# Kernel tuning notes

Hardware: AMD Instinct MI355X
Metric: run time of the kernel (lower is better)

Reference implementation:

```python
import jax, jax.numpy as jnp
import numpy as np

D_MODEL = 1024
KEY_MODEL = 1024
D_K = 64
D_V = 64
N_HEAD = 8
PROJ = N_HEAD * D_V  # 512


def setup_inputs() -> dict:
    key = jax.random.key(0)
    ks = jax.random.split(key, 9)
    N, M = 8192, 8192
    s = 0.02
    return {
        "q": jax.random.normal(ks[0], (N, D_MODEL), jnp.float32),
        "k": jax.random.normal(ks[1], (M, KEY_MODEL), jnp.float32),
        "v": jax.random.normal(ks[2], (M, D_MODEL), jnp.float32),
        "Wq": jax.random.normal(ks[3], (D_MODEL, PROJ), jnp.float32) * s,
        "bq": jnp.zeros((PROJ,), jnp.float32),
        "Wk": jax.random.normal(ks[4], (KEY_MODEL, PROJ), jnp.float32) * s,
        "bk": jnp.zeros((PROJ,), jnp.float32),
        "Wv": jax.random.normal(ks[5], (D_MODEL, PROJ), jnp.float32) * s,
        "bv": jnp.zeros((PROJ,), jnp.float32),
    }


def reference(q, k, v, Wq, bq, Wk, bk, Wv, bv):
    # Linear projections (torch nn.Linear: x @ W^T + b; here W stored as [in,out])
    qp = q @ Wq + bq                      # [N, PROJ]
    kp = k @ Wk + bk                      # [M, PROJ]
    vp = v @ Wv + bv                      # [M, PROJ]
    # Note: original scales by d_k (NOT sqrt(d_k)); dropout is identity at eval.
    scores = (qp @ kp.T) / D_K            # [N, M]
    attn = jax.nn.softmax(scores, axis=-1)
    return attn @ vp                      # [N, PROJ]
```

## Files before the change

kernel.cpp:

```cpp
#include <hip/hip_runtime.h>
#include <hip/hip_bf16.h>
#include <stdint.h>
#include <stddef.h>

typedef unsigned short u16;
typedef short bf16x8 __attribute__((ext_vector_type(8)));
typedef short bf16x4 __attribute__((ext_vector_type(4)));
typedef float floatx4 __attribute__((ext_vector_type(4)));

#define N_ROWS 8192
#define D_MODEL 1024
#define PROJ 512
#define MHALF 4096
#define SCALE_LOG2E_DK 0.022542110013890054f

__device__ __forceinline__ float bf2f(u16 u) {
    union { unsigned int i; float f; } x; x.i = ((unsigned int)u) << 16; return x.f;
}
__device__ __forceinline__ u16 f2bf(float f) {
    __hip_bfloat16 h = __float2bfloat16(f);
    return *reinterpret_cast<u16*>(&h);
}

__global__ void transpose_w_kernel(const float* __restrict__ in, u16* __restrict__ out,
                                   int R, int C) {
    __shared__ u16 tile[32][33];
    int r = blockIdx.y * 32 + threadIdx.y;
    int c = blockIdx.x * 32 + threadIdx.x;
    tile[threadIdx.y][threadIdx.x] = f2bf(in[(size_t)r * C + c]);
    __syncthreads();
    int ro = blockIdx.x * 32 + threadIdx.y;
    int co = blockIdx.y * 32 + threadIdx.x;
    out[(size_t)ro * R + co] = tile[threadIdx.x][threadIdx.y];
}

__global__ void transpose_kernel(const u16* __restrict__ in, u16* __restrict__ out,
                                 int R, int C) {
    __shared__ u16 tile[32][33];
    int r = blockIdx.y * 32 + threadIdx.y;
    int c = blockIdx.x * 32 + threadIdx.x;
    tile[threadIdx.y][threadIdx.x] = in[(size_t)r * C + c];
    __syncthreads();
    int ro = blockIdx.x * 32 + threadIdx.y;
    int co = blockIdx.y * 32 + threadIdx.x;
    out[(size_t)ro * R + co] = tile[threadIdx.x][threadIdx.y];
}

__global__ __launch_bounds__(256) void proj_kernel(
    const float* __restrict__ qin, const float* __restrict__ kin, const float* __restrict__ vin,
    const u16* __restrict__ WqT, const u16* __restrict__ WkT, const u16* __restrict__ WvT,
    const float* __restrict__ bq, const float* __restrict__ bk, const float* __restrict__ bv,
    u16* __restrict__ qp, u16* __restrict__ kp, u16* __restrict__ vp)
{
    const int z = blockIdx.z;
    const float* A    = (z == 0) ? qin : (z == 1) ? kin : vin;
    const u16* WT     = (z == 0) ? WqT : (z == 1) ? WkT : WvT;
    const float* bias = (z == 0) ? bq  : (z == 1) ? bk  : bv;
    u16* C            = (z == 0) ? qp  : (z == 1) ? kp  : vp;

    const int m0 = blockIdx.x * 128;
    const int n0 = blockIdx.y * 128;
    __shared__ __align__(16) u16 smem[2 * 128 * 40];
    u16* As = smem;
    u16* Bs = smem + 128 * 40;

    const int t = threadIdx.x;
    const int w = t >> 6, l = t & 63;
    const int q16 = l >> 4, l16 = l & 15;
    const int wm = (w & 1) * 64, wn = (w >> 1) * 64;

    floatx4 acc[4][4] = {};

    for (int k0 = 0; k0 < D_MODEL; k0 += 32) {
        __syncthreads();
#pragma unroll
        for (int i = 0; i < 4; ++i) {
            int id = i * 256 + t;
            int r = id >> 3, c = id & 7;
            float4 f = *(const float4*)(A + (size_t)(m0 + r) * D_MODEL + k0 + c * 4);
            bf16x4 hv;
            hv[0] = (short)f2bf(f.x); hv[1] = (short)f2bf(f.y);
            hv[2] = (short)f2bf(f.z); hv[3] = (short)f2bf(f.w);
            *(bf16x4*)(As + r * 40 + c * 4) = hv;
        }
#pragma unroll
        for (int i = 0; i < 2; ++i) {
            int id = i * 256 + t;
            int r = id >> 2, c = id & 3;
            *(bf16x8*)(Bs + r * 40 + c * 8) =
                *(const bf16x8*)(WT + (size_t)(n0 + r) * D_MODEL + k0 + c * 8);
        }
        __syncthreads();

        bf16x8 af[4], bfr[4];
#pragma unroll
        for (int mi = 0; mi < 4; ++mi)
            af[mi] = *(const bf16x8*)(As + (wm + mi * 16 + l16) * 40 + q16 * 8);
#pragma unroll
        for (int ni = 0; ni < 4; ++ni)
            bfr[ni] = *(const bf16x8*)(Bs + (wn + ni * 16 + l16) * 40 + q16 * 8);
#pragma unroll
        for (int mi = 0; mi < 4; ++mi)
#pragma unroll
            for (int ni = 0; ni < 4; ++ni)
                acc[mi][ni] = __builtin_amdgcn_mfma_f32_16x16x32_bf16(
                    af[mi], bfr[ni], acc[mi][ni], 0, 0, 0);
    }

#pragma unroll
    for (int ni = 0; ni < 4; ++ni) {
        int col = n0 + wn + ni * 16 + l16;
        float bv_ = bias[col];
#pragma unroll
        for (int mi = 0; mi < 4; ++mi)
#pragma unroll
            for (int rr = 0; rr < 4; ++rr) {
                int row = m0 + wm + mi * 16 + q16 * 4 + rr;
                C[(size_t)row * PROJ + col] = f2bf(acc[mi][ni][rr] + bv_);
            }
    }
}

__global__ void zero_l_kernel(float* __restrict__ l) {
    l[blockIdx.x * 256 + threadIdx.x] = 0.f;
}

__global__ __launch_bounds__(256) void score_kernel(
    const u16* __restrict__ qp, const u16* __restrict__ kph,
    u16* __restrict__ P, float* __restrict__ l)
{
    const int m0 = blockIdx.x * 128;
    const int n0 = blockIdx.y * 128;
    __shared__ __align__(16) u16 smem[2 * 128 * 40];
    u16* As = smem;
    u16* Bs = smem + 128 * 40;

    const int t = threadIdx.x;
    const int w = t >> 6, lane = t & 63;
    const int q16 = lane >> 4, l16 = lane & 15;
    const int wm = (w & 1) * 64, wn = (w >> 1) * 64;

    floatx4 acc[4][4] = {};

    for (int k0 = 0; k0 < PROJ; k0 += 32) {
        __syncthreads();
#pragma unroll
        for (int i = 0; i < 2; ++i) {
            int id = i * 256 + t;
            int r = id >> 2, c = id & 3;
            *(bf16x8*)(As + r * 40 + c * 8) =
                *(const bf16x8*)(qp + (size_t)(m0 + r) * PROJ + k0 + c * 8);
            *(bf16x8*)(Bs + r * 40 + c * 8) =
                *(const bf16x8*)(kph + (size_t)(n0 + r) * PROJ + k0 + c * 8);
        }
        __syncthreads();

        bf16x8 af[4], bfr[4];
#pragma unroll
        for (int mi = 0; mi < 4; ++mi)
            af[mi] = *(const bf16x8*)(As + (wm + mi * 16 + l16) * 40 + q16 * 8);
#pragma unroll
        for (int ni = 0; ni < 4; ++ni)
            bfr[ni] = *(const bf16x8*)(Bs + (wn + ni * 16 + l16) * 40 + q16 * 8);
#pragma unroll
        for (int mi = 0; mi < 4; ++mi)
#pragma unroll
            for (int ni = 0; ni < 4; ++ni)
                acc[mi][ni] = __builtin_amdgcn_mfma_f32_16x16x32_bf16(
                    af[mi], bfr[ni], acc[mi][ni], 0, 0, 0);
    }

#pragma unroll
    for (int mi = 0; mi < 4; ++mi)
#pragma unroll
        for (int rr = 0; rr < 4; ++rr) {
            int row = m0 + wm + mi * 16 + q16 * 4 + rr;
            u16* Prow = P + (size_t)row * MHALF + n0 + wn;
            float tot = 0.f;
#pragma unroll
            for (int ni = 0; ni < 4; ++ni) {
                float x = acc[mi][ni][rr] * SCALE_LOG2E_DK;
                x = fminf(fmaxf(x, -30.f), 30.f);
                float p = exp2f(x);
                tot += p;
                Prow[ni * 16 + l16] = f2bf(p);
            }
#pragma unroll
            for (int m = 1; m < 16; m <<= 1)
                tot += __shfl_xor(tot, m, 64);
            if (l16 == 0)
                atomicAdd(&l[row], tot);
        }
}

__global__ __launch_bounds__(256) void pv_kernel(
    const u16* __restrict__ P, const u16* __restrict__ vpTh,
    float* __restrict__ Ofull, u16* __restrict__ Opart, int accum)
{
    const int m0 = blockIdx.x * 128;
    const int n0 = blockIdx.y * 128;
    const int kg = blockIdx.z;
    const int kbase = kg * 2048;
    __shared__ __align__(16) u16 smem[2 * 128 * 40];
    u16* As = smem;
    u16* Bs = smem + 128 * 40;

    const int t = threadIdx.x;
    const int w = t >> 6, lane = t & 63;
    const int q16 = lane >> 4, l16 = lane & 15;
    const int wm = (w & 1) * 64, wn = (w >> 1) * 64;

    floatx4 acc[4][4] = {};

    for (int kk = 0; kk < 2048; kk += 32) {
        const int k0 = kbase + kk;
        __syncthreads();
#pragma unroll
        for (int i = 0; i < 2; ++i) {
            int id = i * 256 + t;
            int r = id >> 2, c = id & 3;
            *(bf16x8*)(As + r * 40 + c * 8) =
                *(const bf16x8*)(P + (size_t)(m0 + r) * MHALF + k0 + c * 8);
            *(bf16x8*)(Bs + r * 40 + c * 8) =
                *(const bf16x8*)(vpTh + (size_t)(n0 + r) * N_ROWS + k0 + c * 8);
        }
        __syncthreads();

        bf16x8 af[4], bfr[4];
#pragma unroll
        for (int mi = 0; mi < 4; ++mi)
            af[mi] = *(const bf16x8*)(As + (wm + mi * 16 + l16) * 40 + q16 * 8);
#pragma unroll
        for (int ni = 0; ni < 4; ++ni)
            bfr[ni] = *(const bf16x8*)(Bs + (wn + ni * 16 + l16) * 40 + q16 * 8);
#pragma unroll
        for (int mi = 0; mi < 4; ++mi)
#pragma unroll
            for (int ni = 0; ni < 4; ++ni)
                acc[mi][ni] = __builtin_amdgcn_mfma_f32_16x16x32_bf16(
                    af[mi], bfr[ni], acc[mi][ni], 0, 0, 0);
    }

#pragma unroll
    for (int ni = 0; ni < 4; ++ni) {
        int col = n0 + wn + ni * 16 + l16;
#pragma unroll
        for (int mi = 0; mi < 4; ++mi)
#pragma unroll
            for (int rr = 0; rr < 4; ++rr) {
                int row = m0 + wm + mi * 16 + q16 * 4 + rr;
                size_t o = (size_t)row * PROJ + col;
                float v = acc[mi][ni][rr];
                if (kg == 0) {
                    if (accum) v += Ofull[o];
                    Ofull[o] = v;
                } else {
                    if (accum) v += bf2f(Opart[o]);
                    Opart[o] = f2bf(v);
                }
            }
    }
}

__global__ void scale_kernel(float* __restrict__ out, const u16* __restrict__ Opart,
                             const float* __restrict__ l)
{
    int idx = blockIdx.x * 256 + threadIdx.x;
    int row = idx >> 9;
    out[idx] = (out[idx] + bf2f(Opart[idx])) / l[row];
}

extern "C" void kernel_launch(void* const* d_in, const int* in_sizes, int n_in,
                              void* d_out, int out_size, void* d_ws, size_t ws_size,
                              hipStream_t stream)
{
    (void)in_sizes; (void)n_in; (void)out_size;
    if (ws_size < ((size_t)101 << 20)) return;

    const float* q  = (const float*)d_in[0];
    const float* k  = (const float*)d_in[1];
    const float* v  = (const float*)d_in[2];
    const float* Wq = (const float*)d_in[3];
    const float* bq = (const float*)d_in[4];
    const float* Wk = (const float*)d_in[5];
    const float* bk = (const float*)d_in[6];
    const float* Wv = (const float*)d_in[7];
    const float* bv = (const float*)d_in[8];

    char* ws = (char*)d_ws;
    u16* qp    = (u16*)(ws);
    u16* kp    = (u16*)(ws + ((size_t)8  << 20));
    u16* vp    = (u16*)(ws + ((size_t)16 << 20));
    u16* vpT   = (u16*)(ws + ((size_t)24 << 20));
    u16* WqT   = (u16*)(ws + ((size_t)32 << 20));
    u16* WkT   = (u16*)(ws + ((size_t)33 << 20));
    u16* WvT   = (u16*)(ws + ((size_t)34 << 20));
    float* l   = (float*)(ws + ((size_t)35 << 20));
    u16* P     = (u16*)(ws + ((size_t)36 << 20));
    u16* Opart = vp;
    float* Ofull = (float*)d_out;

    dim3 tb(32, 32);
    transpose_w_kernel<<<dim3(16, 32), tb, 0, stream>>>(Wq, WqT, 1024, 512);
    transpose_w_kernel<<<dim3(16, 32), tb, 0, stream>>>(Wk, WkT, 1024, 512);
    transpose_w_kernel<<<dim3(16, 32), tb, 0, stream>>>(Wv, WvT, 1024, 512);

    proj_kernel<<<dim3(64, 4, 3), 256, 0, stream>>>(q, k, v, WqT, WkT, WvT,
                                                    bq, bk, bv, qp, kp, vp);

    transpose_kernel<<<dim3(16, 256), tb, 0, stream>>>(vp, vpT, 8192, 512);

    zero_l_kernel<<<32, 256, 0, stream>>>(l);

    score_kernel<<<dim3(64, 32), 256, 0, stream>>>(qp, kp, P, l);
    pv_kernel<<<dim3(64, 4, 2), 256, 0, stream>>>(P, vpT, Ofull, Opart, 0);
    score_kernel<<<dim3(64, 32), 256, 0, stream>>>(qp, kp + (size_t)MHALF * PROJ, P, l);
    pv_kernel<<<dim3(64, 4, 2), 256, 0, stream>>>(P, vpT + MHALF, Ofull, Opart, 1);

    scale_kernel<<<16384, 256, 0, stream>>>(Ofull, Opart, l);
}
```

Before: 454.2 us.

## Stage GEMM tiles via direct global-to-LDS loads and pre-convert inputs to bf16

Adds a separate kernel that converts q, k and v from fp32 to bf16 into workspace. The projection GEMM now reads bf16 inputs. All three GEMM kernels stage their tiles with the global_load_lds builtin, which writes directly into unpadded 32-wide LDS rows instead of going through registers. This removes register round-trips and in-loop conversion, but adds an extra full pass over the inputs. The unpadded LDS layout may cause bank conflicts on the fragment reads.

```diff
diff --git a/kernel.cpp b/kernel.cpp
--- a/kernel.cpp
+++ b/kernel.cpp
@@ -5,7 +5,6 @@
 
 typedef unsigned short u16;
 typedef short bf16x8 __attribute__((ext_vector_type(8)));
-typedef short bf16x4 __attribute__((ext_vector_type(4)));
 typedef float floatx4 __attribute__((ext_vector_type(4)));
 
 #define N_ROWS 8192
@@ -20,6 +19,24 @@
 __device__ __forceinline__ u16 f2bf(float f) {
     __hip_bfloat16 h = __float2bfloat16(f);
     return *reinterpret_cast<u16*>(&h);
+}
+
+__device__ __forceinline__ void gload_lds16(u16* lds_base, const u16* g) {
+    __builtin_amdgcn_global_load_lds(
+        (const __attribute__((address_space(1))) void*)g,
+        (__attribute__((address_space(3))) void*)lds_base,
+        16, 0, 0);
+}
+
+__device__ __forceinline__ void stage128x32(u16* lds, const u16* src, int stride,
+                                            int wv, int ln) {
+    const int rr = ln >> 2;
+    const int cc = (ln & 3) << 3;
+#pragma unroll
+    for (int i = 0; i < 2; ++i) {
+        const int rb = i * 64 + wv * 16;
+        gload_lds16(lds + rb * 32, src + (size_t)(rb + rr) * stride + cc);
+    }
 }
 
 __global__ void transpose_w_kernel(const float* __restrict__ in, u16* __restrict__ out,
@@ -46,59 +63,61 @@
     out[(size_t)ro * R + co] = tile[threadIdx.x][threadIdx.y];
 }
 
+__global__ __launch_bounds__(256) void convert_bf16_kernel(
+    const float* __restrict__ q, const float* __restrict__ k, const float* __restrict__ v,
+    u16* __restrict__ qb, u16* __restrict__ kb, u16* __restrict__ vb)
+{
+    const float* in = (blockIdx.y == 0) ? q : (blockIdx.y == 1) ? k : v;
+    u16* out        = (blockIdx.y == 0) ? qb : (blockIdx.y == 1) ? kb : vb;
+    size_t i = ((size_t)blockIdx.x * 256 + threadIdx.x) * 8;
+    float4 a = *(const float4*)(in + i);
+    float4 b = *(const float4*)(in + i + 4);
+    bf16x8 o;
+    o[0] = (short)f2bf(a.x); o[1] = (short)f2bf(a.y);
+    o[2] = (short)f2bf(a.z); o[3] = (short)f2bf(a.w);
+    o[4] = (short)f2bf(b.x); o[5] = (short)f2bf(b.y);
+    o[6] = (short)f2bf(b.z); o[7] = (short)f2bf(b.w);
+    *(bf16x8*)(out + i) = o;
+}
+
 __global__ __launch_bounds__(256) void proj_kernel(
-    const float* __restrict__ qin, const float* __restrict__ kin, const float* __restrict__ vin,
+    const u16* __restrict__ qb, const u16* __restrict__ kb, const u16* __restrict__ vb,
     const u16* __restrict__ WqT, const u16* __restrict__ WkT, const u16* __restrict__ WvT,
     const float* __restrict__ bq, const float* __restrict__ bk, const float* __restrict__ bv,
     u16* __restrict__ qp, u16* __restrict__ kp, u16* __restrict__ vp)
 {
     const int z = blockIdx.z;
-    const float* A    = (z == 0) ? qin : (z == 1) ? kin : vin;
+    const u16* A      = (z == 0) ? qb  : (z == 1) ? kb  : vb;
     const u16* WT     = (z == 0) ? WqT : (z == 1) ? WkT : WvT;
     const float* bias = (z == 0) ? bq  : (z == 1) ? bk  : bv;
     u16* C            = (z == 0) ? qp  : (z == 1) ? kp  : vp;
 
     const int m0 = blockIdx.x * 128;
     const int n0 = blockIdx.y * 128;
-    __shared__ __align__(16) u16 smem[2 * 128 * 40];
+    __shared__ __align__(16) u16 smem[2 * 128 * 32];
     u16* As = smem;
-    u16* Bs = smem + 128 * 40;
+    u16* Bs = smem + 128 * 32;
 
     const int t = threadIdx.x;
-    const int w = t >> 6, l = t & 63;
-    const int q16 = l >> 4, l16 = l & 15;
-    const int wm = (w & 1) * 64, wn = (w >> 1) * 64;
+    const int wv = t >> 6, ln = t & 63;
+    const int q16 = ln >> 4, l16 = ln & 15;
+    const int wm = (wv & 1) * 64, wn = (wv >> 1) * 64;
 
     floatx4 acc[4][4] = {};
 
     for (int k0 = 0; k0 < D_MODEL; k0 += 32) {
         __syncthreads();
-#pragma unroll
-        for (int i = 0; i < 4; ++i) {
-            int id = i * 256 + t;
-            int r = id >> 3, c = id & 7;
-            float4 f = *(const float4*)(A + (size_t)(m0 + r) * D_MODEL + k0 + c * 4);
-            bf16x4 hv;
-            hv[0] = (short)f2bf(f.x); hv[1] = (short)f2bf(f.y);
-            hv[2] = (short)f2bf(f.z); hv[3] = (short)f2bf(f.w);
-            *(bf16x4*)(As + r * 40 + c * 4) = hv;
-        }
-#pragma unroll
-        for (int i = 0; i < 2; ++i) {
-            int id = i * 256 + t;
-            int r = id >> 2, c = id & 3;
-            *(bf16x8*)(Bs + r * 40 + c * 8) =
-                *(const bf16x8*)(WT + (size_t)(n0 + r) * D_MODEL + k0 + c * 8);
-        }
+        stage128x32(As, A  + (size_t)m0 * D_MODEL + k0, D_MODEL, wv, ln);
+        stage128x32(Bs, WT + (size_t)n0 * D_MODEL + k0, D_MODEL, wv, ln);
         __syncthreads();
 
         bf16x8 af[4], bfr[4];
 #pragma unroll
         for (int mi = 0; mi < 4; ++mi)
-            af[mi] = *(const bf16x8*)(As + (wm + mi * 16 + l16) * 40 + q16 * 8);
+            af[mi] = *(const bf16x8*)(As + (wm + mi * 16 + l16) * 32 + q16 * 8);
 #pragma unroll
         for (int ni = 0; ni < 4; ++ni)
-            bfr[ni] = *(const bf16x8*)(Bs + (wn + ni * 16 + l16) * 40 + q16 * 8);
+            bfr[ni] = *(const bf16x8*)(Bs + (wn + ni * 16 + l16) * 32 + q16 * 8);
 #pragma unroll
         for (int mi = 0; mi < 4; ++mi)
 #pragma unroll
@@ -131,37 +150,30 @@
 {
     const int m0 = blockIdx.x * 128;
     const int n0 = blockIdx.y * 128;
-    __shared__ __align__(16) u16 smem[2 * 128 * 40];
+    __shared__ __align__(16) u16 smem[2 * 128 * 32];
     u16* As = smem;
-    u16* Bs = smem + 128 * 40;
+    u16* Bs = smem + 128 * 32;
 
     const int t = threadIdx.x;
-    const int w = t >> 6, lane = t & 63;
-    const int q16 = lane >> 4, l16 = lane & 15;
-    const int wm = (w & 1) * 64, wn = (w >> 1) * 64;
+    const int wv = t >> 6, ln = t & 63;
+    const int q16 = ln >> 4, l16 = ln & 15;
+    const int wm = (wv & 1) * 64, wn = (wv >> 1) * 64;
 
     floatx4 acc[4][4] = {};
 
     for (int k0 = 0; k0 < PROJ; k0 += 32) {
         __syncthreads();
-#pragma unroll
-        for (int i = 0; i < 2; ++i) {
-            int id = i * 256 + t;
-            int r = id >> 2, c = id & 3;
-            *(bf16x8*)(As + r * 40 + c * 8) =
-                *(const bf16x8*)(qp + (size_t)(m0 + r) * PROJ + k0 + c * 8);
-            *(bf16x8*)(Bs + r * 40 + c * 8) =
-                *(const bf16x8*)(kph + (size_t)(n0 + r) * PROJ + k0 + c * 8);
-        }
+        stage128x32(As, qp  + (size_t)m0 * PROJ + k0, PROJ, wv, ln);
+        stage128x32(Bs, kph + (size_t)n0 * PROJ + k0, PROJ, wv, ln);
         __syncthreads();
 
         bf16x8 af[4], bfr[4];
 #pragma unroll
         for (int mi = 0; mi < 4; ++mi)
-            af[mi] = *(const bf16x8*)(As + (wm + mi * 16 + l16) * 40 + q16 * 8);
+            af[mi] = *(const bf16x8*)(As + (wm + mi * 16 + l16) * 32 + q16 * 8);
 #pragma unroll
         for (int ni = 0; ni < 4; ++ni)
-            bfr[ni] = *(const bf16x8*)(Bs + (wn + ni * 16 + l16) * 40 + q16 * 8);
+            bfr[ni] = *(const bf16x8*)(Bs + (wn + ni * 16 + l16) * 32 + q16 * 8);
 #pragma unroll
         for (int mi = 0; mi < 4; ++mi)
 #pragma unroll
@@ -201,38 +213,31 @@
     const int n0 = blockIdx.y * 128;
     const int kg = blockIdx.z;
     const int kbase = kg * 2048;
-    __shared__ __align__(16) u16 smem[2 * 128 * 40];
+    __shared__ __align__(16) u16 smem[2 * 128 * 32];
     u16* As = smem;
-    u16* Bs = smem + 128 * 40;
+    u16* Bs = smem + 128 * 32;
 
     const int t = threadIdx.x;
-    const int w = t >> 6, lane = t & 63;
-    const int q16 = lane >> 4, l16 = lane & 15;
-    const int wm = (w & 1) * 64, wn = (w >> 1) * 64;
+    const int wv = t >> 6, ln = t & 63;
+    const int q16 = ln >> 4, l16 = ln & 15;
+    const int wm = (wv & 1) * 64, wn = (wv >> 1) * 64;
 
     floatx4 acc[4][4] = {};
 
     for (int kk = 0; kk < 2048; kk += 32) {
         const int k0 = kbase + kk;
         __syncthreads();
-#pragma unroll
-        for (int i = 0; i < 2; ++i) {
-            int id = i * 256 + t;
-            int r = id >> 2, c = id & 3;
-            *(bf16x8*)(As + r * 40 + c * 8) =
-                *(const bf16x8*)(P + (size_t)(m0 + r) * MHALF + k0 + c * 8);
-            *(bf16x8*)(Bs + r * 40 + c * 8) =
-                *(const bf16x8*)(vpTh + (size_t)(n0 + r) * N_ROWS + k0 + c * 8);
-        }
+        stage128x32(As, P    + (size_t)m0 * MHALF  + k0, MHALF,  wv, ln);
+        stage128x32(Bs, vpTh + (size_t)n0 * N_ROWS + k0, N_ROWS, wv, ln);
         __syncthreads();
 
         bf16x8 af[4], bfr[4];
 #pragma unroll
         for (int mi = 0; mi < 4; ++mi)
-            af[mi] = *(const bf16x8*)(As + (wm + mi * 16 + l16) * 40 + q16 * 8);
+            af[mi] = *(const bf16x8*)(As + (wm + mi * 16 + l16) * 32 + q16 * 8);
 #pragma unroll
         for (int ni = 0; ni < 4; ++ni)
-            bfr[ni] = *(const bf16x8*)(Bs + (wn + ni * 16 + l16) * 40 + q16 * 8);
+            bfr[ni] = *(const bf16x8*)(Bs + (wn + ni * 16 + l16) * 32 + q16 * 8);
 #pragma unroll
         for (int mi = 0; mi < 4; ++mi)
 #pragma unroll
@@ -297,6 +302,9 @@
     u16* WvT   = (u16*)(ws + ((size_t)34 << 20));
     float* l   = (float*)(ws + ((size_t)35 << 20));
     u16* P     = (u16*)(ws + ((size_t)36 << 20));
+    u16* qb    = (u16*)(ws + ((size_t)36 << 20));
+    u16* kb    = (u16*)(ws + ((size_t)52 << 20));
+    u16* vb    = (u16*)(ws + ((size_t)68 << 20));
     u16* Opart = vp;
     float* Ofull = (float*)d_out;
 
@@ -305,7 +313,9 @@
     transpose_w_kernel<<<dim3(16, 32), tb, 0, stream>>>(Wk, WkT, 1024, 512);
     transpose_w_kernel<<<dim3(16, 32), tb, 0, stream>>>(Wv, WvT, 1024, 512);
 
-    proj_kernel<<<dim3(64, 4, 3), 256, 0, stream>>>(q, k, v, WqT, WkT, WvT,
+    convert_bf16_kernel<<<dim3(4096, 3), 256, 0, stream>>>(q, k, v, qb, kb, vb);
+
+    proj_kernel<<<dim3(64, 4, 3), 256, 0, stream>>>(qb, kb, vb, WqT, WkT, WvT,
                                                     bq, bk, bv, qp, kp, vp);
 
     transpose_kernel<<<dim3(16, 256), tb, 0, stream>>>(vp, vpT, 8192, 512);
```

New measurement: 425.9 us. -6.2%, faster.
